# Kernel tuning notes

Hardware: AMD Instinct MI355X
Metric: run time of the kernel (lower is better)

The kernel has to match this reference:

```python
import jax, jax.numpy as jnp
import numpy as np

B, T, IN, HID, OUT = 64, 250, 1024, 2048, 256
TAU_TRACE = 20.0
TAU_MEM = 20.0
THR = 1.0
LR = 1e-4
WD = 0.01
DECAY_TRACE = float(np.exp(-1.0 / TAU_TRACE))
ALPHA = float(np.exp(-1.0 / TAU_MEM))


def _spike(v):
    # Heaviside spike with straight-through sigmoid surrogate gradient
    sur = jax.nn.sigmoid(4.0 * (v - THR))
    hard = (v > THR).astype(v.dtype)
    return sur + jax.lax.stop_gradient(hard - sur)


def _lif(current, v):
    # leaky integrate-and-fire with soft reset
    v = ALPHA * v + current
    z = _spike(v)
    v = v - z * THR
    return z, v


def _exp_convolve(spk, trace, decay):
    return decay * trace + (1.0 - decay) * spk


def _stdp(pre_trace, post_trace, w):
    # delta_w = lr * (batch-mean post x pre outer product - weight decay), detached
    outer = jnp.einsum('bo,bi->oi', post_trace, pre_trace) / pre_trace.shape[0]
    return jax.lax.stop_gradient(LR * (outer - WD * w))


def setup_inputs() -> dict:
    key = jax.random.key(0)
    k1, k2, k3 = jax.random.split(key, 3)
    x = (jax.random.uniform(k1, (B, T, IN)) < 0.1).astype(jnp.float32)  # spike raster
    input_weight = jax.random.uniform(k2, (HID, IN), dtype=jnp.float32)
    hidden_weight = jax.random.uniform(k3, (OUT, HID), dtype=jnp.float32)
    return {"x": x, "input_weight": input_weight, "hidden_weight": hidden_weight, "train": 1}


def reference(x, input_weight, hidden_weight, train):
    b = x.shape[0]
    dt = x.dtype
    v1 = jnp.zeros((b, HID), dt)
    v2 = jnp.zeros((b, OUT), dt)
    l1_tr = jnp.zeros((b, HID), dt)
    l2_tr = jnp.zeros((b, OUT), dt)
    in_tr = jnp.zeros((b, IN), dt)
    xs = jnp.swapaxes(x, 0, 1)  # [T, B, IN]

    if train:
        def step(carry, spk):
            w_in, w_hid, in_tr, l1_tr, l2_tr, v1, v2 = carry
            in_tr = _exp_convolve(spk, in_tr, DECAY_TRACE)
            l1, v1 = _lif(0.2 * (spk @ w_in.T), v1)
            l1_tr = _exp_convolve(l1, l1_tr, DECAY_TRACE)
            l2, v2 = _lif(0.2 * (l1 @ w_hid.T), v2)
            l2_tr = _exp_convolve(l2, l2_tr, DECAY_TRACE)
            w_in = w_in + _stdp(in_tr, l1_tr, w_in)
            w_hid = w_hid + _stdp(l1_tr, l2_tr, w_hid)
            return (w_in, w_hid, in_tr, l1_tr, l2_tr, v1, v2), (l1, l2)

        carry0 = (input_weight, hidden_weight, in_tr, l1_tr, l2_tr, v1, v2)
        carry, (l1s, l2s) = jax.lax.scan(step, carry0, xs)
        _, _, _, l1_tr, l2_tr, v1, v2 = carry
    else:
        def step(carry, spk):
            in_tr, v1, v2 = carry
            in_tr = _exp_convolve(spk, in_tr, DECAY_TRACE)
            l1, v1 = _lif(0.2 * (spk @ input_weight.T), v1)
            l2, v2 = _lif(0.2 * (l1 @ hidden_weight.T), v2)
            return (in_tr, v1, v2), (l1, l2)

        (_, v1, v2), (l1s, l2s) = jax.lax.scan(step, (in_tr, v1, v2), xs)

    l1_seq = jnp.swapaxes(l1s, 0, 1)  # [B, T, HID]
    l2_seq = jnp.swapaxes(l2s, 0, 1)  # [B, T, OUT]
    return l1_seq, l2_seq, v1, v2, l1_tr, l2_tr
```

## Files before the change

### kernel.cpp

```cpp
#include <hip/hip_runtime.h>
#include <hip/hip_cooperative_groups.h>
#include <stdint.h>

namespace cg = cooperative_groups;

#define BB   64
#define TTT  250
#define INN  1024
#define HIDD 2048
#define OUTT 256

#define DECAYF 0.951229424500714f
#define ALPHAF 0.951229424500714f
#define LRF    1e-4f
#define WDF    0.01f
#define SCLF   0.2f

#define O_L1SEQ 0
#define O_L2SEQ 32768000
#define O_V1    36864000
#define O_V2    36995072
#define O_L1TR  37011456
#define O_L2TR  37142528

#define CH  3
#define NPH 84

#define WS_XBITS 0
#define WS_INTRT 73728
#define WS_L1BIT 1253376
#define WS_L1TT  1351680
#define WS_FLAG  2924544

#define NB1 64
#define NB2 16
#define NBLK 80
#define NTHR 512

typedef __attribute__((ext_vector_type(8))) short short8v;
typedef __attribute__((ext_vector_type(4))) float float4v;

__device__ inline short f2bf(float f) {
  union { float f; uint32_t u; } c; c.f = f;
  uint32_t u = c.u + 0x7fffu + ((c.u >> 16) & 1u);
  return (short)(u >> 16);
}

__device__ inline short8v expand8(uint32_t byte) {
  union { uint32_t u[4]; short8v v; } r;
#pragma unroll
  for (int p2 = 0; p2 < 4; p2++) {
    r.u[p2] = (((byte >> (2 * p2)) & 1u) ? 0x3F80u : 0u) |
              (((byte >> (2 * p2 + 1)) & 1u) ? 0x3F800000u : 0u);
  }
  return r.v;
}

__device__ inline void bar_lds() {
  asm volatile("s_waitcnt lgkmcnt(0)\n\ts_barrier" ::: "memory");
}

__device__ inline int ldf(int* p) {
  return __hip_atomic_load(p, __ATOMIC_RELAXED, __HIP_MEMORY_SCOPE_AGENT);
}
__device__ inline void postflag(int* p) {
  __hip_atomic_fetch_add(p, 1, __ATOMIC_RELEASE, __HIP_MEMORY_SCOPE_AGENT);
}
__device__ inline void postflag_rx(int* p) {
  __hip_atomic_fetch_add(p, 1, __ATOMIC_RELAXED, __HIP_MEMORY_SCOPE_AGENT);
}

__device__ inline int swz1024(int row, int k) {
  return row * 1024 + ((((k) >> 3) ^ (row & 7)) << 3) + ((k) & 7);
}
__device__ inline int swz2048(int row, int k) {
  return row * 2048 + ((((k) >> 3) ^ (row & 7)) << 3) + ((k) & 7);
}
__device__ inline int swz64(int row, int k) {
  return row * 64 + ((((k) >> 3) ^ (row & 7)) << 3) + ((k) & 7);
}

struct SG1 {
  short winb[32 * 1024];
  float v1s[64 * 33];
  float l1trs[64 * 33];
  short l1trT[32 * 64];
  float red[2048];
};
struct SG2 {
  short whb[16 * 2048];
  float v2s[64 * 17];
  float l2trs[64 * 17];
  short l2trT[16 * 64];
  float red[4 * 256];
};

__global__ __launch_bounds__(NTHR, 1) void kmain(const float* __restrict__ x,
                                                 const float* __restrict__ w_in,
                                                 const float* __restrict__ w_hid,
                                                 float* __restrict__ out,
                                                 char* __restrict__ ws) {
  __shared__ __align__(16) char smem[94720];
  cg::grid_group grid = cg::this_grid();
  const int bid = blockIdx.x, tid = threadIdx.x;
  const int lane = tid & 63, wv = tid >> 6;
  const int mr = lane & 15, q = lane >> 4;

  int* FB = (int*)(ws + WS_FLAG);
  int* FP = FB;
  int* FE = FB + 128;
  int* FL2 = FB + 256;

  if (bid == 0) for (int c = tid; c < 384; c += NTHR) FB[c] = 0;
  grid.sync();

  if (bid < NB1) {
    SG1& S = *(SG1*)smem;
    const int h0 = bid * 32;
    const int btw = wv & 3, kh = wv >> 2;
    float wreg[64];
    const int ia = wv * 128 + lane, ib2 = ia + 64;
    float itra = 0.f, itrb = 0.f;

#pragma unroll
    for (int j = 0; j < 8; j++) {
      const int i = (wv * 8 + j) * 16 + mr;
#pragma unroll
      for (int ht2 = 0; ht2 < 2; ht2++)
#pragma unroll
        for (int r = 0; r < 4; r++) {
          const int hl = ht2 * 16 + q * 4 + r;
          float w = w_in[(h0 + hl) * INN + i];
          wreg[(j * 2 + ht2) * 4 + r] = w;
          S.winb[swz1024(hl, i)] = f2bf(w);
        }
    }
    for (int c = tid; c < 64 * 33; c += NTHR) { S.v1s[c] = 0.f; S.l1trs[c] = 0.f; }
    for (int s = 0; s < CH; s++) {
      float xa = x[(bid * TTT + s) * INN + ia];
      float xb2 = x[(bid * TTT + s) * INN + ib2];
      itra = DECAYF * itra + (1.f - DECAYF) * xa;
      itrb = DECAYF * itrb + (1.f - DECAYF) * xb2;
      short* intT = (short*)(ws + WS_INTRT) + s * (INN * BB);
      intT[ia * 64 + bid] = f2bf(itra);
      intT[ib2 * 64 + bid] = f2bf(itrb);
      unsigned long long balA = __ballot(xa > 0.5f);
      unsigned long long balB = __ballot(xb2 > 0.5f);
      if (lane == 0) {
        uint32_t* xbw = (uint32_t*)(ws + WS_XBITS) + s * (BB * 32) + bid * 32 + wv * 4;
        xbw[0] = (uint32_t)balA; xbw[1] = (uint32_t)(balA >> 32);
        xbw[2] = (uint32_t)balB; xbw[3] = (uint32_t)(balB >> 32);
      }
    }
    __syncthreads();
    if (tid == 0) postflag(&FP[0]);

    for (int p = 0; p < NPH; p++) {
      const int t0 = p * CH;
      const int ns = (TTT - t0 < CH) ? (TTT - t0) : CH;
      if (tid == 0) {
        for (;;) {
          int a = ldf(&FP[p]);
          int b2 = (p >= 2) ? ldf(&FE[p - 2]) : 64;
          int c2 = (p >= 2) ? ldf(&FL2[p - 2]) : 16;
          if (a >= 64 && b2 >= 64 && c2 >= 16) break;
        }
        __threadfence();
      }
      bar_lds();

      for (int s = 0; s < ns; s++) {
        const int t = t0 + s;
        const uint32_t* xbw = (const uint32_t*)(ws + WS_XBITS) +
                              ((p % 3) * CH + s) * (BB * 32);
        float4v acc0 = {0.f, 0.f, 0.f, 0.f}, acc1 = acc0;
        {
          const uint32_t* brow = xbw + (btw * 16 + mr) * 32 + kh * 16;
#pragma unroll 8
          for (int ks = 0; ks < 16; ks++) {
            const int koff = ks * 32 + q * 8;
            short8v af = expand8(brow[ks] >> (q * 8));
            short8v bf0 = *(const short8v*)&S.winb[swz1024(mr, kh * 512 + koff)];
            short8v bf1 = *(const short8v*)&S.winb[swz1024(16 + mr, kh * 512 + koff)];
            acc0 = __builtin_amdgcn_mfma_f32_16x16x32_bf16(af, bf0, acc0, 0, 0, 0);
            acc1 = __builtin_amdgcn_mfma_f32_16x16x32_bf16(af, bf1, acc1, 0, 0, 0);
          }
        }
        if (kh == 1) {
          *(float4v*)&S.red[(btw * 2 + 0) * 256 + lane * 4] = acc0;
          *(float4v*)&S.red[(btw * 2 + 1) * 256 + lane * 4] = acc1;
        }
        bar_lds();

        short* l1ttg = (short*)(ws + WS_L1TT) + ((p & 1) * CH + s) * (HIDD * BB);
        if (kh == 0) {
          const int b0 = btw * 16 + q * 4;
          float zf0[4], zf1[4];
#pragma unroll
          for (int ht2 = 0; ht2 < 2; ht2++) {
            float4v ac = ht2 ? acc1 : acc0;
            float4v o4 = *(const float4v*)&S.red[(btw * 2 + ht2) * 256 + lane * 4];
            const int hl = ht2 * 16 + mr, h = h0 + hl;
            short trs[4];
#pragma unroll
            for (int r = 0; r < 4; r++) {
              const int b = b0 + r;
              float v = ALPHAF * S.v1s[b * 33 + hl] + SCLF * (ac[r] + o4[r]);
              float z = v > 1.0f ? 1.0f : 0.0f;
              v -= z;
              S.v1s[b * 33 + hl] = v;
              out[O_L1SEQ + (b * TTT + t) * HIDD + h] = z;
              if (ht2 == 0) zf0[r] = z; else zf1[r] = z;
              float tr = DECAYF * S.l1trs[b * 33 + hl] + (1.f - DECAYF) * z;
              S.l1trs[b * 33 + hl] = tr;
              short tb = f2bf(tr);
              S.l1trT[swz64(hl, b)] = tb;
              trs[r] = tb;
            }
            *(short4*)(l1ttg + h * 64 + b0) = *(short4*)trs;
          }
          uint32_t* l1bw = (uint32_t*)(ws + WS_L1BIT) + ((p & 1) * CH + s) * (BB * 64);
#pragma unroll
          for (int r = 0; r < 4; r++) {
            unsigned long long bal0 = __ballot(zf0[r] > 0.5f);
            unsigned long long bal1 = __ballot(zf1[r] > 0.5f);
            if (mr == 0) {
              uint32_t w0 = (uint32_t)((bal0 >> (q * 16)) & 0xFFFFull);
              uint32_t w1 = (uint32_t)((bal1 >> (q * 16)) & 0xFFFFull);
              l1bw[(b0 + r) * 64 + bid] = w0 | (w1 << 16);
            }
          }
        }
        bar_lds();

        {
          const short* intT = (const short*)(ws + WS_INTRT) + ((p % 3) * CH + s) * (INN * BB);
#pragma unroll
          for (int j = 0; j < 8; j++) {
            const int it = wv * 8 + j;
            float4v a20 = {0.f, 0.f, 0.f, 0.f}, a21 = a20;
#pragma unroll
            for (int ks = 0; ks < 2; ks++) {
              const int koff = ks * 32 + q * 8;
              short8v bf = *(const short8v*)(intT + (it * 16 + mr) * 64 + koff);
              short8v af0 = *(const short8v*)&S.l1trT[swz64(mr, koff)];
              short8v af1 = *(const short8v*)&S.l1trT[swz64(16 + mr, koff)];
              a20 = __builtin_amdgcn_mfma_f32_16x16x32_bf16(af0, bf, a20, 0, 0, 0);
              a21 = __builtin_amdgcn_mfma_f32_16x16x32_bf16(af1, bf, a21, 0, 0, 0);
            }
            const int i = it * 16 + mr;
#pragma unroll
            for (int ht2 = 0; ht2 < 2; ht2++) {
              float4v a2 = ht2 ? a21 : a20;
#pragma unroll
              for (int r = 0; r < 4; r++) {
                const int hl = ht2 * 16 + q * 4 + r;
                const int widx = (j * 2 + ht2) * 4 + r;
                float w = wreg[widx] * (1.f - LRF * WDF) + (LRF / 64.f) * a2[r];
                wreg[widx] = w;
                S.winb[swz1024(hl, i)] = f2bf(w);
              }
            }
          }
        }
        bar_lds();

        if (s == 0 && p + 1 < NPH) {
          const int pt0 = (p + 1) * CH, pp = (p + 1) % 3;
          for (int s2 = 0; s2 < CH && pt0 + s2 < TTT; s2++) {
            float xa = x[(bid * TTT + pt0 + s2) * INN + ia];
            float xb2 = x[(bid * TTT + pt0 + s2) * INN + ib2];
            itra = DECAYF * itra + (1.f - DECAYF) * xa;
            itrb = DECAYF * itrb + (1.f - DECAYF) * xb2;
            short* intTn = (short*)(ws + WS_INTRT) + (pp * CH + s2) * (INN * BB);
            intTn[ia * 64 + bid] = f2bf(itra);
            intTn[ib2 * 64 + bid] = f2bf(itrb);
            unsigned long long balA = __ballot(xa > 0.5f);
            unsigned long long balB = __ballot(xb2 > 0.5f);
            if (lane == 0) {
              uint32_t* xbwn = (uint32_t*)(ws + WS_XBITS) + (pp * CH + s2) * (BB * 32) +
                               bid * 32 + wv * 4;
              xbwn[0] = (uint32_t)balA; xbwn[1] = (uint32_t)(balA >> 32);
              xbwn[2] = (uint32_t)balB; xbwn[3] = (uint32_t)(balB >> 32);
            }
          }
          __syncthreads();
          if (tid == 0) postflag(&FP[p + 1]);
        }
      }
      __syncthreads();
      if (tid == 0) postflag(&FE[p]);
    }
    for (int c = tid; c < 64 * 32; c += NTHR) {
      const int b = c >> 5, hl = c & 31;
      out[O_V1 + b * HIDD + h0 + hl] = S.v1s[b * 33 + hl];
      out[O_L1TR + b * HIDD + h0 + hl] = S.l1trs[b * 33 + hl];
    }
  } else {
    SG2& S = *(SG2*)smem;
    const int o0 = (bid - NB1) * 16;
    const int bt = wv & 3, kh = wv >> 2;
    float wreg[64];

#pragma unroll
    for (int j = 0; j < 16; j++) {
      const int hcol = (wv * 16 + j) * 16 + mr;
#pragma unroll
      for (int r = 0; r < 4; r++) {
        const int ol = q * 4 + r;
        float w = w_hid[(o0 + ol) * HIDD + hcol];
        wreg[j * 4 + r] = w;
        S.whb[swz2048(ol, hcol)] = f2bf(w);
      }
    }
    for (int c = tid; c < 64 * 17; c += NTHR) { S.v2s[c] = 0.f; S.l2trs[c] = 0.f; }

    for (int p = 0; p < NPH; p++) {
      const int t0 = p * CH;
      const int ns = (TTT - t0 < CH) ? (TTT - t0) : CH;
      if (tid == 0) {
        while (ldf(&FE[p]) < 64) {}
        __threadfence();
      }
      bar_lds();

      for (int s = 0; s < ns; s++) {
        const int u = t0 + s;
        const uint32_t* l1bw = (const uint32_t*)(ws + WS_L1BIT) +
                               ((p & 1) * CH + s) * (BB * 64);
        float4v acc = {0.f, 0.f, 0.f, 0.f};
        {
          const uint32_t* brow = l1bw + (bt * 16 + mr) * 64 + kh * 32;
#pragma unroll 8
          for (int ks = 0; ks < 32; ks++) {
            const int kk = kh * 1024 + ks * 32 + q * 8;
            short8v af = expand8(brow[ks] >> (q * 8));
            short8v bf = *(const short8v*)&S.whb[swz2048(mr, kk)];
            acc = __builtin_amdgcn_mfma_f32_16x16x32_bf16(af, bf, acc, 0, 0, 0);
          }
        }
        if (kh == 1) { *(float4v*)&S.red[bt * 256 + lane * 4] = acc; }
        bar_lds();
        if (kh == 0) {
          float4v o4 = *(const float4v*)&S.red[bt * 256 + lane * 4];
#pragma unroll
          for (int r = 0; r < 4; r++) {
            const int b = bt * 16 + q * 4 + r;
            float v = ALPHAF * S.v2s[b * 17 + mr] + SCLF * (acc[r] + o4[r]);
            float z = v > 1.0f ? 1.0f : 0.0f;
            v -= z;
            S.v2s[b * 17 + mr] = v;
            out[O_L2SEQ + (b * TTT + u) * OUTT + o0 + mr] = z;
            float tr = DECAYF * S.l2trs[b * 17 + mr] + (1.f - DECAYF) * z;
            S.l2trs[b * 17 + mr] = tr;
            S.l2trT[swz64(mr, b)] = f2bf(tr);
          }
        }
        bar_lds();

        {
          const short* l1ttg = (const short*)(ws + WS_L1TT) + ((p & 1) * CH + s) * (HIDD * BB);
#pragma unroll
          for (int j = 0; j < 16; j++) {
            const int htile = wv * 16 + j;
            float4v a2 = {0.f, 0.f, 0.f, 0.f};
#pragma unroll
            for (int ks = 0; ks < 2; ks++) {
              const int koff = ks * 32 + q * 8;
              short8v af = *(const short8v*)&S.l2trT[swz64(mr, koff)];
              short8v bf = *(const short8v*)(l1ttg + (htile * 16 + mr) * 64 + koff);
              a2 = __builtin_amdgcn_mfma_f32_16x16x32_bf16(af, bf, a2, 0, 0, 0);
            }
            const int hcol = htile * 16 + mr;
#pragma unroll
            for (int r = 0; r < 4; r++) {
              const int ol = q * 4 + r;
              float w = wreg[j * 4 + r] * (1.f - LRF * WDF) + (LRF / 64.f) * a2[r];
              wreg[j * 4 + r] = w;
              S.whb[swz2048(ol, hcol)] = f2bf(w);
            }
          }
        }
        bar_lds();
      }
      if (tid == 0) postflag_rx(&FL2[p]);
    }
    for (int c = tid; c < 64 * 16; c += NTHR) {
      const int b = c >> 4, ol = c & 15;
      out[O_V2 + b * OUTT + o0 + ol] = S.v2s[b * 17 + ol];
      out[O_L2TR + b * OUTT + o0 + ol] = S.l2trs[b * 17 + ol];
    }
  }
}

extern "C" void kernel_launch(void* const* d_in, const int* in_sizes, int n_in,
                              void* d_out, int out_size, void* d_ws, size_t ws_size,
                              hipStream_t stream) {
  const float* x = (const float*)d_in[0];
  const float* w_in = (const float*)d_in[1];
  const float* w_hid = (const float*)d_in[2];
  float* out = (float*)d_out;
  char* ws = (char*)d_ws;

  void* args[] = {(void*)&x, (void*)&w_in, (void*)&w_hid, (void*)&out, (void*)&ws};
  hipLaunchCooperativeKernel(reinterpret_cast<void*>(kmain), dim3(NBLK), dim3(NTHR),
                             args, 0, stream);
}
```

Baseline: 3.402 ms.

## Double block threads to 1024 with 4-way K split and sleep in spin-waits

Doubles threads per block from 512 to 1024. The forward matmul K dimension is now split four ways across wave groups instead of two, with a larger LDS reduction buffer. The per-wave weight register slices and STDP update tiles are halved, which lowers per-thread work and register pressure in the persistent cooperative kernel. Adds s_sleep inside the flag spin loops to reduce polling pressure, at the cost of more reduction traffic and possibly slower wake-up.

New measurement: 3.929 ms. +15.5%, slower.

```diff
diff --git a/kernel.cpp b/kernel.cpp
--- a/kernel.cpp
+++ b/kernel.cpp
@@ -35,7 +35,7 @@
 #define NB1 64
 #define NB2 16
 #define NBLK 80
-#define NTHR 512
+#define NTHR 1024
 
 typedef __attribute__((ext_vector_type(8))) short short8v;
 typedef __attribute__((ext_vector_type(4))) float float4v;
@@ -85,14 +85,14 @@
   float v1s[64 * 33];
   float l1trs[64 * 33];
   short l1trT[32 * 64];
-  float red[2048];
+  float red[24 * 256];
 };
 struct SG2 {
   short whb[16 * 2048];
   float v2s[64 * 17];
   float l2trs[64 * 17];
   short l2trT[16 * 64];
-  float red[4 * 256];
+  float red[12 * 256];
 };
 
 __global__ __launch_bounds__(NTHR, 1) void kmain(const float* __restrict__ x,
@@ -100,7 +100,7 @@
                                                  const float* __restrict__ w_hid,
                                                  float* __restrict__ out,
                                                  char* __restrict__ ws) {
-  __shared__ __align__(16) char smem[94720];
+  __shared__ __align__(16) char smem[111104];
   cg::grid_group grid = cg::this_grid();
   const int bid = blockIdx.x, tid = threadIdx.x;
   const int lane = tid & 63, wv = tid >> 6;
@@ -117,14 +117,14 @@
   if (bid < NB1) {
     SG1& S = *(SG1*)smem;
     const int h0 = bid * 32;
-    const int btw = wv & 3, kh = wv >> 2;
-    float wreg[64];
-    const int ia = wv * 128 + lane, ib2 = ia + 64;
-    float itra = 0.f, itrb = 0.f;
-
-#pragma unroll
-    for (int j = 0; j < 8; j++) {
-      const int i = (wv * 8 + j) * 16 + mr;
+    const int btw = wv & 3, kq = wv >> 2;
+    float wreg[32];
+    const int ia = tid;
+    float itra = 0.f;
+
+#pragma unroll
+    for (int j = 0; j < 4; j++) {
+      const int i = (wv * 4 + j) * 16 + mr;
 #pragma unroll
       for (int ht2 = 0; ht2 < 2; ht2++)
 #pragma unroll
@@ -138,18 +138,13 @@
     for (int c = tid; c < 64 * 33; c += NTHR) { S.v1s[c] = 0.f; S.l1trs[c] = 0.f; }
     for (int s = 0; s < CH; s++) {
       float xa = x[(bid * TTT + s) * INN + ia];
-      float xb2 = x[(bid * TTT + s) * INN + ib2];
       itra = DECAYF * itra + (1.f - DECAYF) * xa;
-      itrb = DECAYF * itrb + (1.f - DECAYF) * xb2;
       short* intT = (short*)(ws + WS_INTRT) + s * (INN * BB);
       intT[ia * 64 + bid] = f2bf(itra);
-      intT[ib2 * 64 + bid] = f2bf(itrb);
       unsigned long long balA = __ballot(xa > 0.5f);
-      unsigned long long balB = __ballot(xb2 > 0.5f);
       if (lane == 0) {
-        uint32_t* xbw = (uint32_t*)(ws + WS_XBITS) + s * (BB * 32) + bid * 32 + wv * 4;
+        uint32_t* xbw = (uint32_t*)(ws + WS_XBITS) + s * (BB * 32) + bid * 32 + wv * 2;
         xbw[0] = (uint32_t)balA; xbw[1] = (uint32_t)(balA >> 32);
-        xbw[2] = (uint32_t)balB; xbw[3] = (uint32_t)(balB >> 32);
       }
     }
     __syncthreads();
@@ -164,6 +159,7 @@
           int b2 = (p >= 2) ? ldf(&FE[p - 2]) : 64;
           int c2 = (p >= 2) ? ldf(&FL2[p - 2]) : 16;
           if (a >= 64 && b2 >= 64 && c2 >= 16) break;
+          __builtin_amdgcn_s_sleep(2);
         }
         __threadfence();
       }
@@ -175,37 +171,41 @@
                               ((p % 3) * CH + s) * (BB * 32);
         float4v acc0 = {0.f, 0.f, 0.f, 0.f}, acc1 = acc0;
         {
-          const uint32_t* brow = xbw + (btw * 16 + mr) * 32 + kh * 16;
-#pragma unroll 8
-          for (int ks = 0; ks < 16; ks++) {
-            const int koff = ks * 32 + q * 8;
+          const uint32_t* brow = xbw + (btw * 16 + mr) * 32 + kq * 8;
+#pragma unroll
+          for (int ks = 0; ks < 8; ks++) {
+            const int koff = kq * 256 + ks * 32 + q * 8;
             short8v af = expand8(brow[ks] >> (q * 8));
-            short8v bf0 = *(const short8v*)&S.winb[swz1024(mr, kh * 512 + koff)];
-            short8v bf1 = *(const short8v*)&S.winb[swz1024(16 + mr, kh * 512 + koff)];
+            short8v bf0 = *(const short8v*)&S.winb[swz1024(mr, koff)];
+            short8v bf1 = *(const short8v*)&S.winb[swz1024(16 + mr, koff)];
             acc0 = __builtin_amdgcn_mfma_f32_16x16x32_bf16(af, bf0, acc0, 0, 0, 0);
             acc1 = __builtin_amdgcn_mfma_f32_16x16x32_bf16(af, bf1, acc1, 0, 0, 0);
           }
         }
-        if (kh == 1) {
-          *(float4v*)&S.red[(btw * 2 + 0) * 256 + lane * 4] = acc0;
-          *(float4v*)&S.red[(btw * 2 + 1) * 256 + lane * 4] = acc1;
+        if (kq != 0) {
+          *(float4v*)&S.red[(((btw * 2 + 0) * 3) + (kq - 1)) * 256 + lane * 4] = acc0;
+          *(float4v*)&S.red[(((btw * 2 + 1) * 3) + (kq - 1)) * 256 + lane * 4] = acc1;
         }
         bar_lds();
 
         short* l1ttg = (short*)(ws + WS_L1TT) + ((p & 1) * CH + s) * (HIDD * BB);
-        if (kh == 0) {
+        if (kq == 0) {
           const int b0 = btw * 16 + q * 4;
           float zf0[4], zf1[4];
 #pragma unroll
           for (int ht2 = 0; ht2 < 2; ht2++) {
             float4v ac = ht2 ? acc1 : acc0;
-            float4v o4 = *(const float4v*)&S.red[(btw * 2 + ht2) * 256 + lane * 4];
+            const int rb = (btw * 2 + ht2) * 3;
+            float4v o4 = *(const float4v*)&S.red[(rb + 0) * 256 + lane * 4];
+            float4v o5 = *(const float4v*)&S.red[(rb + 1) * 256 + lane * 4];
+            float4v o6 = *(const float4v*)&S.red[(rb + 2) * 256 + lane * 4];
             const int hl = ht2 * 16 + mr, h = h0 + hl;
             short trs[4];
 #pragma unroll
             for (int r = 0; r < 4; r++) {
               const int b = b0 + r;
-              float v = ALPHAF * S.v1s[b * 33 + hl] + SCLF * (ac[r] + o4[r]);
+              float v = ALPHAF * S.v1s[b * 33 + hl] +
+                        SCLF * (ac[r] + o4[r] + o5[r] + o6[r]);
               float z = v > 1.0f ? 1.0f : 0.0f;
               v -= z;
               S.v1s[b * 33 + hl] = v;
@@ -236,8 +236,8 @@
         {
           const short* intT = (const short*)(ws + WS_INTRT) + ((p % 3) * CH + s) * (INN * BB);
 #pragma unroll
-          for (int j = 0; j < 8; j++) {
-            const int it = wv * 8 + j;
+          for (int j = 0; j < 4; j++) {
+            const int it = wv * 4 + j;
             float4v a20 = {0.f, 0.f, 0.f, 0.f}, a21 = a20;
 #pragma unroll
             for (int ks = 0; ks < 2; ks++) {
@@ -269,19 +269,14 @@
           const int pt0 = (p + 1) * CH, pp = (p + 1) % 3;
           for (int s2 = 0; s2 < CH && pt0 + s2 < TTT; s2++) {
             float xa = x[(bid * TTT + pt0 + s2) * INN + ia];
-            float xb2 = x[(bid * TTT + pt0 + s2) * INN + ib2];
             itra = DECAYF * itra + (1.f - DECAYF) * xa;
-            itrb = DECAYF * itrb + (1.f - DECAYF) * xb2;
             short* intTn = (short*)(ws + WS_INTRT) + (pp * CH + s2) * (INN * BB);
             intTn[ia * 64 + bid] = f2bf(itra);
-            intTn[ib2 * 64 + bid] = f2bf(itrb);
             unsigned long long balA = __ballot(xa > 0.5f);
-            unsigned long long balB = __ballot(xb2 > 0.5f);
             if (lane == 0) {
               uint32_t* xbwn = (uint32_t*)(ws + WS_XBITS) + (pp * CH + s2) * (BB * 32) +
-                               bid * 32 + wv * 4;
+                               bid * 32 + wv * 2;
               xbwn[0] = (uint32_t)balA; xbwn[1] = (uint32_t)(balA >> 32);
-              xbwn[2] = (uint32_t)balB; xbwn[3] = (uint32_t)(balB >> 32);
             }
           }
           __syncthreads();
@@ -299,12 +294,12 @@
   } else {
     SG2& S = *(SG2*)smem;
     const int o0 = (bid - NB1) * 16;
-    const int bt = wv & 3, kh = wv >> 2;
-    float wreg[64];
-
-#pragma unroll
-    for (int j = 0; j < 16; j++) {
-      const int hcol = (wv * 16 + j) * 16 + mr;
+    const int bt = wv & 3, kq = wv >> 2;
+    float wreg[32];
+
+#pragma unroll
+    for (int j = 0; j < 8; j++) {
+      const int hcol = (wv * 8 + j) * 16 + mr;
 #pragma unroll
       for (int r = 0; r < 4; r++) {
         const int ol = q * 4 + r;
@@ -319,7 +314,7 @@
       const int t0 = p * CH;
       const int ns = (TTT - t0 < CH) ? (TTT - t0) : CH;
       if (tid == 0) {
-        while (ldf(&FE[p]) < 64) {}
+        while (ldf(&FE[p]) < 64) { __builtin_amdgcn_s_sleep(2); }
         __threadfence();
       }
       bar_lds();
@@ -330,23 +325,27 @@
                                ((p & 1) * CH + s) * (BB * 64);
         float4v acc = {0.f, 0.f, 0.f, 0.f};
         {
-          const uint32_t* brow = l1bw + (bt * 16 + mr) * 64 + kh * 32;
-#pragma unroll 8
-          for (int ks = 0; ks < 32; ks++) {
-            const int kk = kh * 1024 + ks * 32 + q * 8;
+          const uint32_t* brow = l1bw + (bt * 16 + mr) * 64 + kq * 16;
+#pragma unroll
+          for (int ks = 0; ks < 16; ks++) {
+            const int kk = kq * 512 + ks * 32 + q * 8;
             short8v af = expand8(brow[ks] >> (q * 8));
             short8v bf = *(const short8v*)&S.whb[swz2048(mr, kk)];
             acc = __builtin_amdgcn_mfma_f32_16x16x32_bf16(af, bf, acc, 0, 0, 0);
           }
         }
-        if (kh == 1) { *(float4v*)&S.red[bt * 256 + lane * 4] = acc; }
-        bar_lds();
-        if (kh == 0) {
-          float4v o4 = *(const float4v*)&S.red[bt * 256 + lane * 4];
+        if (kq != 0) { *(float4v*)&S.red[(bt * 3 + (kq - 1)) * 256 + lane * 4] = acc; }
+        bar_lds();
+        if (kq == 0) {
+          const int rb = bt * 3;
+          float4v o4 = *(const float4v*)&S.red[(rb + 0) * 256 + lane * 4];
+          float4v o5 = *(const float4v*)&S.red[(rb + 1) * 256 + lane * 4];
+          float4v o6 = *(const float4v*)&S.red[(rb + 2) * 256 + lane * 4];
 #pragma unroll
           for (int r = 0; r < 4; r++) {
             const int b = bt * 16 + q * 4 + r;
-            float v = ALPHAF * S.v2s[b * 17 + mr] + SCLF * (acc[r] + o4[r]);
+            float v = ALPHAF * S.v2s[b * 17 + mr] +
+                      SCLF * (acc[r] + o4[r] + o5[r] + o6[r]);
             float z = v > 1.0f ? 1.0f : 0.0f;
             v -= z;
             S.v2s[b * 17 + mr] = v;
@@ -361,8 +360,8 @@
         {
           const short* l1ttg = (const short*)(ws + WS_L1TT) + ((p & 1) * CH + s) * (HIDD * BB);
 #pragma unroll
-          for (int j = 0; j < 16; j++) {
-            const int htile = wv * 16 + j;
+          for (int j = 0; j < 8; j++) {
+            const int htile = wv * 8 + j;
             float4v a2 = {0.f, 0.f, 0.f, 0.f};
 #pragma unroll
             for (int ks = 0; ks < 2; ks++) {
```
